# Kernel tuning notes

Hardware: AMD Instinct MI355X
Metric: run time of the kernel (lower is better)

Reference implementation:

```python
import jax, jax.numpy as jnp
import numpy as np

C = 128

def setup_inputs() -> dict:
    key = jax.random.key(0)
    ks = jax.random.split(key, 7)
    x = jax.random.normal(ks[0], (4, 64, 64, C), dtype=jnp.float32)
    s = 1.0 / np.sqrt(C)
    Wq = jax.random.normal(ks[1], (C, C), dtype=jnp.float32) * s
    bq = jnp.zeros((C,), dtype=jnp.float32)
    Wk = jax.random.normal(ks[2], (C, C), dtype=jnp.float32) * s
    bk = jnp.zeros((C,), dtype=jnp.float32)
    Wv = jax.random.normal(ks[3], (C, C), dtype=jnp.float32) * s
    bv = jnp.zeros((C,), dtype=jnp.float32)
    return {"x": x, "Wq": Wq, "bq": bq, "Wk": Wk, "bk": bk, "Wv": Wv, "bv": bv}

def reference(x, Wq, bq, Wk, bk, Wv, bv):
    B, H, W, Cc = x.shape
    N = H * W
    xt = x.reshape(B, N, Cc)  # 1x1 conv == per-token linear
    q = xt @ Wq + bq
    k = xt @ Wk + bk
    v = xt @ Wv + bv
    scale = jnp.sqrt(jnp.asarray(Cc, dtype=x.dtype))
    attn = jnp.einsum('bnc,bmc->bnm', q, k) / scale  # [B, N, N]
    attn = jax.nn.softmax(attn, axis=-1)
    out = jnp.einsum('bnm,bmc->bnc', attn, v)
    return x + out.reshape(B, H, W, Cc)
```

## Files before the change

kernel.cpp:

```cpp
#include <hip/hip_runtime.h>

constexpr int C       = 128;
constexpr int N       = 4096;
constexpr int BATCH   = 4;
constexpr int TOTROWS = BATCH * N;
constexpr float SCALE = 0.08838834764831845f;
constexpr float LOG2E = 1.44269504088896340736f;

constexpr int BK = 64;

typedef __attribute__((ext_vector_type(8))) short        bf16x8;
typedef __attribute__((ext_vector_type(4))) float        f32x4;
typedef __attribute__((ext_vector_type(2))) unsigned int u32x2;

__device__ inline unsigned short f2bf(float f) {
    unsigned int u = __float_as_uint(f);
    return (unsigned short)((u + 0x7FFFu + ((u >> 16) & 1u)) >> 16);
}
__device__ inline unsigned int cvtpk(float a, float b) {
    unsigned int r;
    asm("v_cvt_pk_bf16_f32 %0, %1, %2" : "=v"(r) : "v"(a), "v"(b));
    return r;
}
__device__ inline float bf2f(unsigned int u) {
    return __uint_as_float(u << 16);
}
__device__ inline float fexp2(float x) {
#if __has_builtin(__builtin_amdgcn_exp2f)
    return __builtin_amdgcn_exp2f(x);
#else
    float r; asm("v_exp_f32 %0, %1\n\ts_nop 0" : "=v"(r) : "v"(x)); return r;
#endif
}
__device__ inline void dma16(const void* g, void* l) {
    __builtin_amdgcn_global_load_lds(
        (const __attribute__((address_space(1))) void*)g,
        (__attribute__((address_space(3))) void*)l, 16, 0, 0);
}

__global__ __launch_bounds__(256)
void wprep_kernel(const float* __restrict__ Wq, const float* __restrict__ Wk,
                  const float* __restrict__ Wv, unsigned short* __restrict__ wt)
{
    const int mat = blockIdx.x;
    const float* W = (mat == 0) ? Wq : (mat == 1) ? Wk : Wv;
    const float  s = (mat == 0) ? SCALE * LOG2E : 1.0f;
    unsigned short* dst = wt + mat * 16384;

    const int t  = threadIdx.x;
    const int i0 = t >> 1;
    const int ch = (t & 1) * 64;
    const float4* src = reinterpret_cast<const float4*>(&W[i0 * 128 + ch]);
    const int gsw = ((i0 >> 3) << 3) + (i0 & 7);
    #pragma unroll
    for (int jv = 0; jv < 16; ++jv) {
        float4 a = src[jv];
        float v[4] = { a.x * s, a.y * s, a.z * s, a.w * s };
        #pragma unroll
        for (int e = 0; e < 4; ++e) {
            int o = ch + jv * 4 + e;
            dst[o * 128 + ((((i0 >> 3) ^ ((o >> 2) & 7))) << 3) + (i0 & 7)] =
                f2bf(v[e]);
        }
    }
    (void)gsw;
}

__global__ __launch_bounds__(256, 2)
void qkv_kernel(const float* __restrict__ x, const unsigned short* __restrict__ wt,
                const float* __restrict__ bq, const float* __restrict__ bk,
                const float* __restrict__ bv,
                unsigned short* __restrict__ qo,
                unsigned short* __restrict__ ko,
                unsigned short* __restrict__ vt)
{
    __shared__ __align__(16) unsigned short wl[2][16384];

    const int tid  = threadIdx.x;
    const int lane = tid & 63;
    const int lo   = lane & 15;
    const int quad = lane >> 4;
    const long rowbase = (long)blockIdx.x * 64 + (tid >> 6) * 16;

    bf16x8 xf[4];
    {
        const float4* xr = reinterpret_cast<const float4*>(&x[(rowbase + lo) * C]);
        #pragma unroll
        for (int ks = 0; ks < 4; ++ks) {
            float4 a  = xr[ks * 8 + quad * 2];
            float4 b2 = xr[ks * 8 + quad * 2 + 1];
            union { bf16x8 v; unsigned int u[4]; } cv;
            cv.u[0] = cvtpk(a.x, a.y);
            cv.u[1] = cvtpk(a.z, a.w);
            cv.u[2] = cvtpk(b2.x, b2.y);
            cv.u[3] = cvtpk(b2.z, b2.w);
            xf[ks] = cv.v;
        }
    }

    auto stageW = [&](int mat, int bufi) {
        const char* src = (const char*)(wt + mat * 16384);
        #pragma unroll
        for (int c = 0; c < 8; ++c)
            dma16(src + (c * 256 + tid) * 16, &wl[bufi][(c * 256 + tid) * 8]);
    };

    stageW(0, 0);
    __syncthreads();

    #pragma unroll
    for (int mat = 0; mat < 3; ++mat) {
        if (mat < 2) stageW(mat + 1, (mat + 1) & 1);
        const unsigned short* wb = wl[mat & 1];

        if (mat < 2) {
            f32x4 acc[8] = {};
            #pragma unroll
            for (int ks = 0; ks < 4; ++ks)
                #pragma unroll
                for (int mt = 0; mt < 8; ++mt) {
                    const int rr = mt * 16 + lo;
                    bf16x8 wf = *reinterpret_cast<const bf16x8*>(
                        &wb[rr * 128 + (((ks * 4 + quad) ^ ((rr >> 2) & 7)) << 3)]);
                    acc[mt] = __builtin_amdgcn_mfma_f32_16x16x32_bf16(
                        wf, xf[ks], acc[mt], 0, 0, 0);
                }
            const float* bias = (mat == 0) ? bq : bk;
            const float  s    = (mat == 0) ? SCALE * LOG2E : 1.0f;
            unsigned short* out = (mat == 0) ? qo : ko;
            long row = rowbase + lo;
            #pragma unroll
            for (int mt = 0; mt < 8; ++mt) {
                float4 bb = *reinterpret_cast<const float4*>(&bias[mt * 16 + quad * 4]);
                u32x2 w;
                w[0] = cvtpk(acc[mt][0] + bb.x * s, acc[mt][1] + bb.y * s);
                w[1] = cvtpk(acc[mt][2] + bb.z * s, acc[mt][3] + bb.w * s);
                *reinterpret_cast<u32x2*>(&out[row * C + mt * 16 + quad * 4]) = w;
            }
        } else {
            f32x4 acc[8] = {};
            #pragma unroll
            for (int ks = 0; ks < 4; ++ks)
                #pragma unroll
                for (int ct = 0; ct < 8; ++ct) {
                    const int rr = ct * 16 + lo;
                    bf16x8 wf = *reinterpret_cast<const bf16x8*>(
                        &wb[rr * 128 + (((ks * 4 + quad) ^ ((rr >> 2) & 7)) << 3)]);
                    acc[ct] = __builtin_amdgcn_mfma_f32_16x16x32_bf16(
                        xf[ks], wf, acc[ct], 0, 0, 0);
                }
            const int b = (int)(rowbase >> 12);
            const int nbase = (int)(rowbase & (N - 1));
            const int n0   = nbase + quad * 4;
            const int nblk = n0 >> 6;
            #pragma unroll
            for (int ct = 0; ct < 8; ++ct) {
                int chan = ct * 16 + lo;
                float bb = bv[chan];
                u32x2 w;
                w[0] = cvtpk(acc[ct][0] + bb, acc[ct][1] + bb);
                w[1] = cvtpk(acc[ct][2] + bb, acc[ct][3] + bb);
                *reinterpret_cast<u32x2*>(
                    &vt[(((size_t)b * 64 + nblk) * 128 + chan) * 64 + (n0 & 63)]) = w;
            }
        }
        __syncthreads();
    }
}

__global__ __launch_bounds__(256, 2)
void attn_kernel(const unsigned short* __restrict__ q,
                 const unsigned short* __restrict__ k,
                 const unsigned short* __restrict__ vt,
                 unsigned short* __restrict__ opart,
                 float* __restrict__ lpart)
{
    __shared__ __align__(16) unsigned short smA[17472];
    __shared__ __align__(16) unsigned short smB[16384];
    __shared__ __align__(16) unsigned short smP[4096];

    const int tid  = threadIdx.x;
    const int wv   = tid >> 6;
    const int lane = tid & 63;
    const int lo   = lane & 15;
    const int quad = lane >> 4;

    const int nspl = (int)(gridDim.x >> 7);
    const int id   = blockIdx.x;
    int b, sl, qt;
    if (nspl == 4) {
        b  = (id >> 1) & 3;
        sl = (id & 1) | (((id >> 3) & 1) << 1);
        qt = id >> 4;
    } else {
        b  = (id >> 1) & 3;
        sl = id & 1;
        qt = id >> 3;
    }
    const int NIT  = (N / nspl) / BK;
    const int koff = sl * (N / nspl);

    const int    rowb  = b * N + qt * 128;
    const size_t qrow0 = (size_t)rowb + wv * 32;
    const char* kb8 = (const char*)(k  + ((size_t)b * N + koff) * C);
    const char* vb8 = (const char*)(vt + ((size_t)b * 64 + (koff >> 6)) * (size_t)(128 * 64));

    unsigned short* PW = smP + wv * 1024;

    bf16x8 qf[2][4];
    #pragma unroll
    for (int nt = 0; nt < 2; ++nt)
        #pragma unroll
        for (int ks = 0; ks < 4; ++ks)
            qf[nt][ks] = *reinterpret_cast<const bf16x8*>(
                &q[(qrow0 + nt * 16 + lo) * C + ks * 32 + quad * 8]);

    int offK[4], offV[4];
    #pragma unroll
    for (int c = 0; c < 4; ++c) {
        int G  = (wv * 4 + c) * 64 + lane;
        int kr = G >> 4;
        offK[c] = kr * 256 + (((G & 15) ^ (kr & 7)) << 4);
        int vr = G >> 3;
        offV[c] = vr * 128 + (((G & 7) ^ (vr & 7)) << 4);
    }

    auto stage = [&](int kt, unsigned short* dstKV) {
        const char* kt8 = kb8 + kt * 16384;
        const char* vt8 = vb8 + kt * 16384;
        #pragma unroll
        for (int c = 0; c < 4; ++c)
            dma16(kt8 + offK[c], dstKV + (wv * 4 + c) * 512);
        #pragma unroll
        for (int c = 0; c < 4; ++c)
            dma16(vt8 + offV[c], dstKV + 8192 + (wv * 4 + c) * 512);
    };

    float l_i[2] = { 0.f, 0.f };
    f32x4 ot[2][8] = {};

    auto body = [&](const unsigned short* base) {
        const unsigned short* kc = base;
        const unsigned short* vc = base + 8192;

        f32x4 st[4][2] = {};
        #pragma unroll
        for (int ks = 0; ks < 4; ++ks)
            #pragma unroll
            for (int mt = 0; mt < 4; ++mt) {
                const bf16x8 kf = *reinterpret_cast<const bf16x8*>(
                    &kc[(mt * 16 + lo) * 128 + (((ks * 4 + quad) ^ (lo & 7)) << 3)]);
                #pragma unroll
                for (int nt = 0; nt < 2; ++nt)
                    st[mt][nt] = __builtin_amdgcn_mfma_f32_16x16x32_bf16(
                        kf, qf[nt][ks], st[mt][nt], 0, 0, 0);
            }

        #pragma unroll
        for (int h = 0; h < 2; ++h) {
            #pragma unroll
            for (int nt = 0; nt < 2; ++nt) {
                const int prow = nt * 16 + lo;
                float ps = 0.f;
                #pragma unroll
                for (int m = 0; m < 2; ++m) {
                    f32x4 s = st[2 * h + m][nt];
                    float p0 = fexp2(s[0]);
                    float p1 = fexp2(s[1]);
                    float p2 = fexp2(s[2]);
                    float p3 = fexp2(s[3]);
                    ps += (p0 + p1) + (p2 + p3);
                    u32x2 w;
                    w[0] = cvtpk(p0, p1);
                    w[1] = cvtpk(p2, p3);
                    *reinterpret_cast<u32x2*>(
                        &PW[prow * 32 + (((2 * m + (quad >> 1)) ^ (prow & 3)) << 3)
                            + (quad & 1) * 4]) = w;
                }
                l_i[nt] += ps;
            }
            bf16x8 pf[2];
            #pragma unroll
            for (int nt = 0; nt < 2; ++nt) {
                const int prow = nt * 16 + lo;
                pf[nt] = *reinterpret_cast<const bf16x8*>(
                    &PW[prow * 32 + ((quad ^ (prow & 3)) << 3)]);
            }
            #pragma unroll
            for (int ct = 0; ct < 8; ++ct) {
                const bf16x8 vf = *reinterpret_cast<const bf16x8*>(
                    &vc[(ct * 16 + lo) * 64 + (((h * 4 + quad) ^ (lo & 7)) << 3)]);
                #pragma unroll
                for (int nt = 0; nt < 2; ++nt)
                    ot[nt][ct] = __builtin_amdgcn_mfma_f32_16x16x32_bf16(
                        vf, pf[nt], ot[nt][ct], 0, 0, 0);
            }
        }
    };

    stage(0, smA);
    __syncthreads();
    for (int kt = 0; kt < NIT; kt += 2) {
        stage(kt + 1, smB);
        body(smA);
        __syncthreads();
        if (kt + 2 < NIT) stage(kt + 2, smA);
        body(smB);
        __syncthreads();
    }

    #pragma unroll
    for (int nt = 0; nt < 2; ++nt) {
        l_i[nt] += __shfl_xor(l_i[nt], 16);
        l_i[nt] += __shfl_xor(l_i[nt], 32);
    }
    if (quad == 0) {
        #pragma unroll
        for (int nt = 0; nt < 2; ++nt)
            lpart[(size_t)sl * TOTROWS + qrow0 + nt * 16 + lo] = l_i[nt];
    }

    constexpr int OSTR = 136;
    unsigned short* obl = smA;
    #pragma unroll
    for (int nt = 0; nt < 2; ++nt) {
        const int row = wv * 32 + nt * 16 + lo;
        #pragma unroll
        for (int ct = 0; ct < 8; ++ct) {
            u32x2 w;
            w[0] = cvtpk(ot[nt][ct][0], ot[nt][ct][1]);
            w[1] = cvtpk(ot[nt][ct][2], ot[nt][ct][3]);
            *reinterpret_cast<u32x2*>(&obl[row * OSTR + ct * 16 + quad * 4]) = w;
        }
    }
    __syncthreads();
    {
        unsigned short* obg = opart + (size_t)sl * TOTROWS * C;
        const int row  = tid >> 1;
        const int half = tid & 1;
        const unsigned short* src = &obl[row * OSTR + half * 64];
        unsigned short*       dst = &obg[((size_t)rowb + row) * C + half * 64];
        #pragma unroll
        for (int i = 0; i < 8; ++i)
            *reinterpret_cast<uint4*>(&dst[i * 8]) =
                *reinterpret_cast<const uint4*>(&src[i * 8]);
    }
}

__global__ __launch_bounds__(256)
void combine_kernel(const float* __restrict__ x,
                    const unsigned short* __restrict__ opart,
                    const float* __restrict__ lpart,
                    float* __restrict__ out, int nspl)
{
    int gid = blockIdx.x * 256 + threadIdx.x;
    int row = gid >> 5;
    int c4  = (gid & 31) * 4;

    float denom = 0.f;
    for (int j = 0; j < nspl; ++j) denom += lpart[(size_t)j * TOTROWS + row];
    float inv = 1.0f / denom;

    size_t idx = (size_t)row * C + c4;
    float a0 = 0.f, a1 = 0.f, a2 = 0.f, a3 = 0.f;
    for (int j = 0; j < nspl; ++j) {
        u32x2 o = *reinterpret_cast<const u32x2*>(
            &opart[(size_t)j * TOTROWS * C + idx]);
        a0 += bf2f(o[0] & 0xffff);
        a1 += bf2f(o[0] >> 16);
        a2 += bf2f(o[1] & 0xffff);
        a3 += bf2f(o[1] >> 16);
    }
    float4 xv = *reinterpret_cast<const float4*>(&x[idx]);
    float4 o;
    o.x = xv.x + a0 * inv;
    o.y = xv.y + a1 * inv;
    o.z = xv.z + a2 * inv;
    o.w = xv.w + a3 * inv;
    *reinterpret_cast<float4*>(&out[idx]) = o;
}

extern "C" void kernel_launch(void* const* d_in, const int* in_sizes, int n_in,
                              void* d_out, int out_size, void* d_ws, size_t ws_size,
                              hipStream_t stream)
{
    const float* x  = (const float*)d_in[0];
    const float* Wq = (const float*)d_in[1];
    const float* bq = (const float*)d_in[2];
    const float* Wk = (const float*)d_in[3];
    const float* bk = (const float*)d_in[4];
    const float* Wv = (const float*)d_in[5];
    const float* bv = (const float*)d_in[6];
    float* out = (float*)d_out;

    const int nspl = (ws_size >= ((size_t)31 << 20)) ? 4 : 2;

    const size_t SPLIT_BYTES = (size_t)TOTROWS * C * 2;
    char* ws = (char*)d_ws;
    unsigned short* opart = (unsigned short*)ws;
    char* base = ws + (size_t)nspl * SPLIT_BYTES;
    unsigned short* q  = (unsigned short*)(base);
    unsigned short* k  = (unsigned short*)(base + SPLIT_BYTES);
    unsigned short* vt = (unsigned short*)(base + 2 * SPLIT_BYTES);
    float*          lp = (float*)(base + 3 * SPLIT_BYTES);
    unsigned short* wt = (unsigned short*)(base + 3 * SPLIT_BYTES
                                           + (size_t)nspl * TOTROWS * 4);

    wprep_kernel<<<3, 256, 0, stream>>>(Wq, Wk, Wv, wt);
    qkv_kernel<<<TOTROWS / 64, 256, 0, stream>>>(x, wt, bq, bk, bv, q, k, vt);
    attn_kernel<<<nspl * 128, 256, 0, stream>>>(q, k, vt, opart, lp);
    combine_kernel<<<TOTROWS * 32 / 256, 256, 0, stream>>>(x, opart, lp, out, nspl);
}
```

Baseline: 132.9 us.

## Fuse split-KV combine into attention kernel via last-block atomic counter

Removes the separate combine kernel. Each attention block bumps a per-(batch, query-tile) atomic counter after writing its partial output, and the last-arriving block reduces all splits, normalizes and adds the residual. A memset of the counters is added to each launch. The weight-prep kernel is also rewritten so each thread writes contiguous 16-byte bf16 groups instead of scattered 2-byte stores. This saves a kernel launch and its tail, but puts the combine work on the last block of each tile, which may lengthen the critical path.

```diff
diff --git a/kernel.cpp b/kernel.cpp
--- a/kernel.cpp
+++ b/kernel.cpp
@@ -48,22 +48,20 @@
     unsigned short* dst = wt + mat * 16384;
 
     const int t  = threadIdx.x;
-    const int i0 = t >> 1;
-    const int ch = (t & 1) * 64;
-    const float4* src = reinterpret_cast<const float4*>(&W[i0 * 128 + ch]);
-    const int gsw = ((i0 >> 3) << 3) + (i0 & 7);
-    #pragma unroll
-    for (int jv = 0; jv < 16; ++jv) {
-        float4 a = src[jv];
-        float v[4] = { a.x * s, a.y * s, a.z * s, a.w * s };
-        #pragma unroll
-        for (int e = 0; e < 4; ++e) {
-            int o = ch + jv * 4 + e;
-            dst[o * 128 + ((((i0 >> 3) ^ ((o >> 2) & 7))) << 3) + (i0 & 7)] =
-                f2bf(v[e]);
-        }
-    }
-    (void)gsw;
+    const int o  = t >> 1;
+    const int g0 = (t & 1) * 8;
+    const int xr = (o >> 2) & 7;
+    #pragma unroll
+    for (int gg = 0; gg < 8; ++gg) {
+        const int g   = g0 + gg;
+        const int ihi = (g & 8) | ((g & 7) ^ xr);
+        const int i0  = ihi << 3;
+        union { unsigned short u16[8]; uint4 v; } buf;
+        #pragma unroll
+        for (int e = 0; e < 8; ++e)
+            buf.u16[e] = f2bf(W[(i0 + e) * 128 + o] * s);
+        *reinterpret_cast<uint4*>(&dst[o * 128 + g * 8]) = buf.v;
+    }
 }
 
 __global__ __launch_bounds__(256, 2)
@@ -173,11 +171,15 @@
                  const unsigned short* __restrict__ k,
                  const unsigned short* __restrict__ vt,
                  unsigned short* __restrict__ opart,
-                 float* __restrict__ lpart)
+                 float* __restrict__ lpart,
+                 const float* __restrict__ x,
+                 float* __restrict__ out,
+                 unsigned int* __restrict__ cnt)
 {
     __shared__ __align__(16) unsigned short smA[17472];
     __shared__ __align__(16) unsigned short smB[16384];
     __shared__ __align__(16) unsigned short smP[4096];
+    __shared__ unsigned int lastflag;
 
     const int tid  = threadIdx.x;
     const int wv   = tid >> 6;
@@ -345,39 +347,47 @@
             *reinterpret_cast<uint4*>(&dst[i * 8]) =
                 *reinterpret_cast<const uint4*>(&src[i * 8]);
     }
-}
-
-__global__ __launch_bounds__(256)
-void combine_kernel(const float* __restrict__ x,
-                    const unsigned short* __restrict__ opart,
-                    const float* __restrict__ lpart,
-                    float* __restrict__ out, int nspl)
-{
-    int gid = blockIdx.x * 256 + threadIdx.x;
-    int row = gid >> 5;
-    int c4  = (gid & 31) * 4;
-
-    float denom = 0.f;
-    for (int j = 0; j < nspl; ++j) denom += lpart[(size_t)j * TOTROWS + row];
-    float inv = 1.0f / denom;
-
-    size_t idx = (size_t)row * C + c4;
-    float a0 = 0.f, a1 = 0.f, a2 = 0.f, a3 = 0.f;
-    for (int j = 0; j < nspl; ++j) {
-        u32x2 o = *reinterpret_cast<const u32x2*>(
-            &opart[(size_t)j * TOTROWS * C + idx]);
-        a0 += bf2f(o[0] & 0xffff);
-        a1 += bf2f(o[0] >> 16);
-        a2 += bf2f(o[1] & 0xffff);
-        a3 += bf2f(o[1] >> 16);
-    }
-    float4 xv = *reinterpret_cast<const float4*>(&x[idx]);
-    float4 o;
-    o.x = xv.x + a0 * inv;
-    o.y = xv.y + a1 * inv;
-    o.z = xv.z + a2 * inv;
-    o.w = xv.w + a3 * inv;
-    *reinterpret_cast<float4*>(&out[idx]) = o;
+
+    __threadfence();
+    __syncthreads();
+    if (tid == 0) {
+        unsigned int old = atomicAdd(&cnt[b * 32 + qt], 1u);
+        lastflag = (old == (unsigned)(nspl - 1)) ? 1u : 0u;
+    }
+    __syncthreads();
+    if (lastflag) {
+        __threadfence();
+        #pragma unroll
+        for (int it = 0; it < 16; ++it) {
+            const int gid  = it * 256 + tid;
+            const int rloc = gid >> 5;
+            const int c4   = (gid & 31) * 4;
+            const size_t row = (size_t)rowb + rloc;
+
+            float denom = 0.f;
+            for (int j = 0; j < nspl; ++j)
+                denom += lpart[(size_t)j * TOTROWS + row];
+            float inv = 1.0f / denom;
+
+            const size_t idx = row * C + c4;
+            float a0 = 0.f, a1 = 0.f, a2 = 0.f, a3 = 0.f;
+            for (int j = 0; j < nspl; ++j) {
+                u32x2 o = *reinterpret_cast<const u32x2*>(
+                    &opart[(size_t)j * TOTROWS * C + idx]);
+                a0 += bf2f(o[0] & 0xffff);
+                a1 += bf2f(o[0] >> 16);
+                a2 += bf2f(o[1] & 0xffff);
+                a3 += bf2f(o[1] >> 16);
+            }
+            float4 xv = *reinterpret_cast<const float4*>(&x[idx]);
+            float4 ov;
+            ov.x = xv.x + a0 * inv;
+            ov.y = xv.y + a1 * inv;
+            ov.z = xv.z + a2 * inv;
+            ov.w = xv.w + a3 * inv;
+            *reinterpret_cast<float4*>(&out[idx]) = ov;
+        }
+    }
 }
 
 extern "C" void kernel_launch(void* const* d_in, const int* in_sizes, int n_in,
@@ -405,9 +415,10 @@
     float*          lp = (float*)(base + 3 * SPLIT_BYTES);
     unsigned short* wt = (unsigned short*)(base + 3 * SPLIT_BYTES
                                            + (size_t)nspl * TOTROWS * 4);
-
+    unsigned int*  cnt = (unsigned int*)((char*)wt + 3 * 16384 * 2);
+
+    hipMemsetAsync(cnt, 0, 128 * sizeof(unsigned int), stream);
     wprep_kernel<<<3, 256, 0, stream>>>(Wq, Wk, Wv, wt);
     qkv_kernel<<<TOTROWS / 64, 256, 0, stream>>>(x, wt, bq, bk, bv, q, k, vt);
-    attn_kernel<<<nspl * 128, 256, 0, stream>>>(q, k, vt, opart, lp);
-    combine_kernel<<<TOTROWS * 32 / 256, 256, 0, stream>>>(x, opart, lp, out, nspl);
-}
+    attn_kernel<<<nspl * 128, 256, 0, stream>>>(q, k, vt, opart, lp, x, out, cnt);
+}
```

Measured after the change: 255.5 us. 92.3% more time.

## Split QKV projection across grid y dimension and vectorize weight prep stores

Applied to the files above, without the earlier changes.

The QKV kernel now launches a 2D grid with one block per (row tile, matrix), so each block loads a single weight matrix into LDS instead of looping over all three with double buffering. This triples the block count, halves LDS per block, and removes the inter-matrix barriers, but each x tile is now read and converted three times. The weight-prep kernel is rewritten so each thread gathers eight values and writes one 16-byte store into the swizzled layout, replacing scattered 2-byte stores.

```diff
diff --git a/kernel.cpp b/kernel.cpp
--- a/kernel.cpp
+++ b/kernel.cpp
@@ -48,22 +48,20 @@
     unsigned short* dst = wt + mat * 16384;
 
     const int t  = threadIdx.x;
-    const int i0 = t >> 1;
-    const int ch = (t & 1) * 64;
-    const float4* src = reinterpret_cast<const float4*>(&W[i0 * 128 + ch]);
-    const int gsw = ((i0 >> 3) << 3) + (i0 & 7);
+    const int o  = t >> 1;
+    const int g0 = (t & 1) * 8;
+    const int xr = (o >> 2) & 7;
     #pragma unroll
-    for (int jv = 0; jv < 16; ++jv) {
-        float4 a = src[jv];
-        float v[4] = { a.x * s, a.y * s, a.z * s, a.w * s };
-        #pragma unroll
-        for (int e = 0; e < 4; ++e) {
-            int o = ch + jv * 4 + e;
-            dst[o * 128 + ((((i0 >> 3) ^ ((o >> 2) & 7))) << 3) + (i0 & 7)] =
-                f2bf(v[e]);
-        }
-    }
-    (void)gsw;
+    for (int gg = 0; gg < 8; ++gg) {
+        const int g   = g0 + gg;
+        const int ihi = (g & 8) | ((g & 7) ^ xr);
+        const int i0  = ihi << 3;
+        union { unsigned short u16[8]; uint4 v; } buf;
+        #pragma unroll
+        for (int e = 0; e < 8; ++e)
+            buf.u16[e] = f2bf(W[(i0 + e) * 128 + o] * s);
+        *reinterpret_cast<uint4*>(&dst[o * 128 + g * 8]) = buf.v;
+    }
 }
 
 __global__ __launch_bounds__(256, 2)
@@ -74,13 +72,21 @@
                 unsigned short* __restrict__ ko,
                 unsigned short* __restrict__ vt)
 {
-    __shared__ __align__(16) unsigned short wl[2][16384];
+    __shared__ __align__(16) unsigned short wl[16384];
 
     const int tid  = threadIdx.x;
     const int lane = tid & 63;
     const int lo   = lane & 15;
     const int quad = lane >> 4;
+    const int mat  = blockIdx.y;
     const long rowbase = (long)blockIdx.x * 64 + (tid >> 6) * 16;
+
+    {
+        const char* src = (const char*)(wt + mat * 16384);
+        #pragma unroll
+        for (int c = 0; c < 8; ++c)
+            dma16(src + (c * 256 + tid) * 16, &wl[(c * 256 + tid) * 8]);
+    }
 
     bf16x8 xf[4];
     {
@@ -98,73 +104,58 @@
         }
     }
 
-    auto stageW = [&](int mat, int bufi) {
-        const char* src = (const char*)(wt + mat * 16384);
-        #pragma unroll
-        for (int c = 0; c < 8; ++c)
-            dma16(src + (c * 256 + tid) * 16, &wl[bufi][(c * 256 + tid) * 8]);
-    };
-
-    stageW(0, 0);
     __syncthreads();
 
-    #pragma unroll
-    for (int mat = 0; mat < 3; ++mat) {
-        if (mat < 2) stageW(mat + 1, (mat + 1) & 1);
-        const unsigned short* wb = wl[mat & 1];
-
-        if (mat < 2) {
-            f32x4 acc[8] = {};
-            #pragma unroll
-            for (int ks = 0; ks < 4; ++ks)
-                #pragma unroll
-                for (int mt = 0; mt < 8; ++mt) {
-                    const int rr = mt * 16 + lo;
-                    bf16x8 wf = *reinterpret_cast<const bf16x8*>(
-                        &wb[rr * 128 + (((ks * 4 + quad) ^ ((rr >> 2) & 7)) << 3)]);
-                    acc[mt] = __builtin_amdgcn_mfma_f32_16x16x32_bf16(
-                        wf, xf[ks], acc[mt], 0, 0, 0);
-                }
-            const float* bias = (mat == 0) ? bq : bk;
-            const float  s    = (mat == 0) ? SCALE * LOG2E : 1.0f;
-            unsigned short* out = (mat == 0) ? qo : ko;
-            long row = rowbase + lo;
+    if (mat < 2) {
+        f32x4 acc[8] = {};
+        #pragma unroll
+        for (int ks = 0; ks < 4; ++ks)
             #pragma unroll
             for (int mt = 0; mt < 8; ++mt) {
-                float4 bb = *reinterpret_cast<const float4*>(&bias[mt * 16 + quad * 4]);
-                u32x2 w;
-                w[0] = cvtpk(acc[mt][0] + bb.x * s, acc[mt][1] + bb.y * s);
-                w[1] = cvtpk(acc[mt][2] + bb.z * s, acc[mt][3] + bb.w * s);
-                *reinterpret_cast<u32x2*>(&out[row * C + mt * 16 + quad * 4]) = w;
-            }
-        } else {
-            f32x4 acc[8] = {};
-            #pragma unroll
-            for (int ks = 0; ks < 4; ++ks)
-                #pragma unroll
-                for (int ct = 0; ct < 8; ++ct) {
-                    const int rr = ct * 16 + lo;
-                    bf16x8 wf = *reinterpret_cast<const bf16x8*>(
-                        &wb[rr * 128 + (((ks * 4 + quad) ^ ((rr >> 2) & 7)) << 3)]);
-                    acc[ct] = __builtin_amdgcn_mfma_f32_16x16x32_bf16(
-                        xf[ks], wf, acc[ct], 0, 0, 0);
-                }
-            const int b = (int)(rowbase >> 12);
-            const int nbase = (int)(rowbase & (N - 1));
-            const int n0   = nbase + quad * 4;
-            const int nblk = n0 >> 6;
+                const int rr = mt * 16 + lo;
+                bf16x8 wf = *reinterpret_cast<const bf16x8*>(
+                    &wl[rr * 128 + (((ks * 4 + quad) ^ ((rr >> 2) & 7)) << 3)]);
+                acc[mt] = __builtin_amdgcn_mfma_f32_16x16x32_bf16(
+                    wf, xf[ks], acc[mt], 0, 0, 0);
+            }
+        const float* bias = (mat == 0) ? bq : bk;
+        const float  s    = (mat == 0) ? SCALE * LOG2E : 1.0f;
+        unsigned short* out = (mat == 0) ? qo : ko;
+        long row = rowbase + lo;
+        #pragma unroll
+        for (int mt = 0; mt < 8; ++mt) {
+            float4 bb = *reinterpret_cast<const float4*>(&bias[mt * 16 + quad * 4]);
+            u32x2 w;
+            w[0] = cvtpk(acc[mt][0] + bb.x * s, acc[mt][1] + bb.y * s);
+            w[1] = cvtpk(acc[mt][2] + bb.z * s, acc[mt][3] + bb.w * s);
+            *reinterpret_cast<u32x2*>(&out[row * C + mt * 16 + quad * 4]) = w;
+        }
+    } else {
+        f32x4 acc[8] = {};
+        #pragma unroll
+        for (int ks = 0; ks < 4; ++ks)
             #pragma unroll
             for (int ct = 0; ct < 8; ++ct) {
-                int chan = ct * 16 + lo;
-                float bb = bv[chan];
-                u32x2 w;
-                w[0] = cvtpk(acc[ct][0] + bb, acc[ct][1] + bb);
-                w[1] = cvtpk(acc[ct][2] + bb, acc[ct][3] + bb);
-                *reinterpret_cast<u32x2*>(
-                    &vt[(((size_t)b * 64 + nblk) * 128 + chan) * 64 + (n0 & 63)]) = w;
-            }
+                const int rr = ct * 16 + lo;
+                bf16x8 wf = *reinterpret_cast<const bf16x8*>(
+                    &wl[rr * 128 + (((ks * 4 + quad) ^ ((rr >> 2) & 7)) << 3)]);
+                acc[ct] = __builtin_amdgcn_mfma_f32_16x16x32_bf16(
+                    xf[ks], wf, acc[ct], 0, 0, 0);
+            }
+        const int b = (int)(rowbase >> 12);
+        const int nbase = (int)(rowbase & (N - 1));
+        const int n0   = nbase + quad * 4;
+        const int nblk = n0 >> 6;
+        #pragma unroll
+        for (int ct = 0; ct < 8; ++ct) {
+            int chan = ct * 16 + lo;
+            float bb = bv[chan];
+            u32x2 w;
+            w[0] = cvtpk(acc[ct][0] + bb, acc[ct][1] + bb);
+            w[1] = cvtpk(acc[ct][2] + bb, acc[ct][3] + bb);
+            *reinterpret_cast<u32x2*>(
+                &vt[(((size_t)b * 64 + nblk) * 128 + chan) * 64 + (n0 & 63)]) = w;
         }
-        __syncthreads();
     }
 }
 
@@ -407,7 +398,8 @@
                                            + (size_t)nspl * TOTROWS * 4);
 
     wprep_kernel<<<3, 256, 0, stream>>>(Wq, Wk, Wv, wt);
-    qkv_kernel<<<TOTROWS / 64, 256, 0, stream>>>(x, wt, bq, bk, bv, q, k, vt);
+    qkv_kernel<<<dim3(TOTROWS / 64, 3), 256, 0, stream>>>(
+        x, wt, bq, bk, bv, q, k, vt);
     attn_kernel<<<nspl * 128, 256, 0, stream>>>(q, k, vt, opart, lp);
     combine_kernel<<<TOTROWS * 32 / 256, 256, 0, stream>>>(x, opart, lp, out, nspl);
 }
```

After: 132.4 us. Within noise of the previous version (-0.3%).
